# Kernel optimization log

Measured on AMD Instinct MI355X. Metric: run time of the kernel, lower is better.

The kernel has to match this reference:

```python
import jax, jax.numpy as jnp
import numpy as np

B, S, F, H, P, O = 512, 336, 16, 256, 48, 1

def _gru_cell(x, h, Wih, Whh, bih, bhh):
    # torch GRU gate order: r, z, n
    gx = x @ Wih.T + bih            # [B, 3H]
    gh = h @ Whh.T + bhh            # [B, 3H]
    rx, zx, nx = jnp.split(gx, 3, axis=-1)
    rh, zh, nh = jnp.split(gh, 3, axis=-1)
    r = jax.nn.sigmoid(rx + rh)
    z = jax.nn.sigmoid(zx + zh)
    n = jnp.tanh(nx + r * nh)
    return (1.0 - z) * n + z * h

def setup_inputs() -> dict:
    key = jax.random.key(0)
    ks = jax.random.split(key, 12)
    s = lambda *sh: 1.0 / np.sqrt(sh[-1])
    d = {}
    d["xb"] = jax.random.normal(ks[0], (B, S, F), dtype=jnp.float32)
    # encoder GRU (1 layer, unidirectional)
    d["enc_Wih"] = jax.random.normal(ks[1], (3 * H, F), dtype=jnp.float32) * s(F)
    d["enc_Whh"] = jax.random.normal(ks[2], (3 * H, H), dtype=jnp.float32) * s(H)
    d["enc_bih"] = jnp.zeros((3 * H,), dtype=jnp.float32)
    d["enc_bhh"] = jnp.zeros((3 * H,), dtype=jnp.float32)
    # attention linear: (H + F) -> S
    d["att_W"] = jax.random.normal(ks[3], (S, H + F), dtype=jnp.float32) * s(H + F)
    d["att_b"] = jnp.zeros((S,), dtype=jnp.float32)
    # decoder GRUCell: input H, hidden H
    d["dec_Wih"] = jax.random.normal(ks[4], (3 * H, H), dtype=jnp.float32) * s(H)
    d["dec_Whh"] = jax.random.normal(ks[5], (3 * H, H), dtype=jnp.float32) * s(H)
    d["dec_bih"] = jnp.zeros((3 * H,), dtype=jnp.float32)
    d["dec_bhh"] = jnp.zeros((3 * H,), dtype=jnp.float32)
    # decoder output: H -> F
    d["out_W"] = jax.random.normal(ks[6], (F, H), dtype=jnp.float32) * s(H)
    d["out_b"] = jnp.zeros((F,), dtype=jnp.float32)
    # final linear: F -> O
    d["lin_W"] = jax.random.normal(ks[7], (O, F), dtype=jnp.float32) * s(F)
    d["lin_b"] = jnp.zeros((O,), dtype=jnp.float32)
    return d

def reference(xb, enc_Wih, enc_Whh, enc_bih, enc_bhh, att_W, att_b,
              dec_Wih, dec_Whh, dec_bih, dec_bhh, out_W, out_b, lin_W, lin_b):
    # ---- encoder: GRU over time ----
    h0 = jnp.zeros((B, H), dtype=xb.dtype)
    xs = jnp.swapaxes(xb, 0, 1)  # [S, B, F]

    def enc_step(h, x):
        h2 = _gru_cell(x, h, enc_Wih, enc_Whh, enc_bih, enc_bhh)
        return h2, h2

    enc_hidden, enc_out = jax.lax.scan(enc_step, h0, xs)
    enc_out = jnp.swapaxes(enc_out, 0, 1)  # [B, S, H]

    # ---- decoder: per-step attention + GRUCell + output proj ----
    y0 = xb[:, -1, :]  # [B, F]

    def dec_step(carry, _):
        h, y = carry
        att_in = jnp.concatenate([h, y], axis=1)          # [B, H+F]
        attn = jax.nn.softmax(att_in @ att_W.T + att_b, axis=-1)  # [B, S]
        combine = jnp.einsum('bs,bsh->bh', attn, enc_out)  # [B, H]
        h2 = _gru_cell(combine, h, dec_Wih, dec_Whh, dec_bih, dec_bhh)
        out = h2 @ out_W.T + out_b                         # [B, F]
        return (h2, out), out

    _, outs = jax.lax.scan(dec_step, (enc_hidden, y0), None, length=P)  # [P, B, F]
    outs = jnp.swapaxes(outs, 0, 1)                        # [B, P, F]
    outs = outs @ lin_W.T + lin_b                          # [B, P, O]
    return outs.squeeze(-1)                                # [B, P]
```

## Files before the change

kernel.cpp:

```cpp
#include <hip/hip_runtime.h>
#include <cstdint>
#include <cstddef>

#define B_ 512
#define S_ 336
#define F_ 16
#define H_ 256
#define P_ 48

typedef __bf16 bhalf;
typedef __attribute__((ext_vector_type(8))) __bf16 bhalf8;
typedef __attribute__((ext_vector_type(4))) float f32x4;

#define MFMA16(A, Bv, C) __builtin_amdgcn_mfma_f32_16x16x32_bf16((A), (Bv), (C), 0, 0, 0)

__device__ __forceinline__ float fastrcp(float x) { return __builtin_amdgcn_rcpf(x); }
__device__ __forceinline__ float sigm(float x) { return fastrcp(1.0f + __expf(-x)); }
__device__ __forceinline__ float tanh_f(float x) { return 2.0f * fastrcp(1.0f + __expf(-2.0f * x)) - 1.0f; }

__device__ __forceinline__ bhalf u16_to_bf(unsigned int u) {
  return __builtin_bit_cast(__bf16, (unsigned short)u);
}
__device__ __forceinline__ unsigned short bf_to_u16(bhalf b) {
  return __builtin_bit_cast(unsigned short, b);
}

__device__ __forceinline__ bhalf8 bzero8() {
  bhalf8 v;
#pragma unroll
  for (int j = 0; j < 8; ++j) v[j] = (bhalf)0.0f;
  return v;
}

__global__ __launch_bounds__(128, 1) void enc_kernel(
    const float* __restrict__ Whh, const float* __restrict__ Wih,
    const float* __restrict__ bih, const float* __restrict__ bhh,
    const float* __restrict__ xb,
    bhalf* __restrict__ enc_out,
    float* __restrict__ hcur,
    unsigned int* __restrict__ hpack,
    unsigned int* __restrict__ flags)
{
  const int tid  = threadIdx.x;
  const int lane = tid & 63;
  const int wv   = tid >> 6;
  const int ncol = lane & 15;
  const int quad = lane >> 4;

  const int blk = blockIdx.x;
  const int g   = (blk & 7) * 4 + (blk >> 6);
  const int w   = (blk >> 3) & 7;
  const int b0  = g * 16;
  const int iw0 = w * 32;
  const int i0  = iw0 + wv * 16;

  bhalf8 bWh[3][9], bWl[3][9];
#pragma unroll
  for (int gg = 0; gg < 3; ++gg) {
    const int jrow = gg * 256 + i0 + ncol;
#pragma unroll
    for (int kt = 0; kt < 9; ++kt) {
      bhalf8 vh = bzero8(), vl = bzero8();
      if (kt < 8) {
        const float* src = Whh + (size_t)jrow * 256 + kt * 32 + quad * 8;
#pragma unroll
        for (int j = 0; j < 8; ++j) {
          const float v = src[j];
          const bhalf h = (bhalf)v;
          vh[j] = h;
          vl[j] = (bhalf)(v - (float)h);
        }
      } else if (quad < 2) {
        const float* src = Wih + (size_t)jrow * 16 + quad * 8;
#pragma unroll
        for (int j = 0; j < 8; ++j) {
          const float v = src[j];
          const bhalf h = (bhalf)v;
          vh[j] = h;
          vl[j] = (bhalf)(v - (float)h);
        }
      }
      bWh[gg][kt] = vh;
      bWl[gg][kt] = vl;
    }
  }

  const int jr = i0 + ncol;
  const float bR  = bih[jr]       + bhh[jr];
  const float bZ  = bih[256 + jr] + bhh[256 + jr];
  const float bNx = bih[512 + jr];
  const float bNh = bhh[512 + jr];

  const int bA = b0 + ncol;
  const int kA = quad * 8;

  float hold[4] = {0.0f, 0.0f, 0.0f, 0.0f};

  for (int t = 0; t < S_; ++t) {
    bhalf8 xh = bzero8(), xl = bzero8();
    if (quad < 2) {
      const float* xp = xb + ((size_t)bA * S_ + t) * F_ + quad * 8;
#pragma unroll
      for (int j = 0; j < 8; ++j) {
        const float v = __builtin_nontemporal_load(xp + j);
        const bhalf h = (bhalf)v;
        xh[j] = h;
        xl[j] = (bhalf)(v - (float)h);
      }
    }

    f32x4 aR0 = {0,0,0,0}, aR1 = {0,0,0,0}, aR2 = {0,0,0,0};
    f32x4 aZ0 = {0,0,0,0}, aZ1 = {0,0,0,0}, aZ2 = {0,0,0,0};
    f32x4 aN0 = {0,0,0,0}, aN1 = {0,0,0,0}, aN2 = {0,0,0,0};
    f32x4 aNx = {0,0,0,0};

    aR0 = MFMA16(xh, bWh[0][8], aR0);
    aR1 = MFMA16(xh, bWl[0][8], aR1);
    aR2 = MFMA16(xl, bWh[0][8], aR2);
    aZ0 = MFMA16(xh, bWh[1][8], aZ0);
    aZ1 = MFMA16(xh, bWl[1][8], aZ1);
    aZ2 = MFMA16(xl, bWh[1][8], aZ2);
    aNx = MFMA16(xh, bWh[2][8], aNx);
    aNx = MFMA16(xh, bWl[2][8], aNx);
    aNx = MFMA16(xl, bWh[2][8], aNx);

    if (t > 0) {
      const unsigned int* fp = &flags[g * 8 + (lane & 7)];
      while (__hip_atomic_load(fp, __ATOMIC_RELAXED, __HIP_MEMORY_SCOPE_AGENT) <
             (unsigned int)t)
        __builtin_amdgcn_s_sleep(1);

      const int slot = (t - 1) & 1;
      const unsigned long long* hp64 =
          (const unsigned long long*)(hpack + ((size_t)slot * B_ + bA) * H_ + kA);

      unsigned long long wbuf[32];
#pragma unroll
      for (int i = 0; i < 32; ++i)
        wbuf[i] = __hip_atomic_load(hp64 + (i >> 2) * 16 + (i & 3),
                                    __ATOMIC_RELAXED, __HIP_MEMORY_SCOPE_AGENT);

#pragma unroll
      for (int kt = 0; kt < 8; ++kt) {
        bhalf8 Ah, Al;
#pragma unroll
        for (int j2 = 0; j2 < 4; ++j2) {
          const unsigned long long w2 = wbuf[kt * 4 + j2];
          Ah[2 * j2]     = u16_to_bf((unsigned int)w2);
          Al[2 * j2]     = u16_to_bf((unsigned int)(w2 >> 16));
          Ah[2 * j2 + 1] = u16_to_bf((unsigned int)(w2 >> 32));
          Al[2 * j2 + 1] = u16_to_bf((unsigned int)(w2 >> 48));
        }
        aR0 = MFMA16(Ah, bWh[0][kt], aR0);
        aR1 = MFMA16(Ah, bWl[0][kt], aR1);
        aR2 = MFMA16(Al, bWh[0][kt], aR2);
        aZ0 = MFMA16(Ah, bWh[1][kt], aZ0);
        aZ1 = MFMA16(Ah, bWl[1][kt], aZ1);
        aZ2 = MFMA16(Al, bWh[1][kt], aZ2);
        aN0 = MFMA16(Ah, bWh[2][kt], aN0);
        aN1 = MFMA16(Ah, bWl[2][kt], aN1);
        aN2 = MFMA16(Al, bWh[2][kt], aN2);
      }
    }

    const int iL = i0 + ncol;
    bhalf his[4];
#pragma unroll
    for (int r = 0; r < 4; ++r) {
      const float sR  = aR0[r] + aR1[r] + aR2[r] + bR;
      const float sZ  = aZ0[r] + aZ1[r] + aZ2[r] + bZ;
      const float nhv = aN0[r] + aN1[r] + aN2[r] + bNh;
      const float nxv = aNx[r] + bNx;
      const float rr = sigm(sR);
      const float zz = sigm(sZ);
      const float nn = tanh_f(nxv + rr * nhv);
      const float h2 = (1.0f - zz) * nn + zz * hold[r];
      hold[r] = h2;
      his[r] = (bhalf)h2;
      const bhalf lo = (bhalf)(h2 - (float)his[r]);
      const int bb = b0 + quad * 4 + r;
      const unsigned int wrd =
          (unsigned int)bf_to_u16(his[r]) | ((unsigned int)bf_to_u16(lo) << 16);
      __hip_atomic_store(&hpack[((size_t)(t & 1) * B_ + bb) * H_ + iL], wrd,
                         __ATOMIC_RELAXED, __HIP_MEMORY_SCOPE_AGENT);
    }

    __syncthreads();
    if (tid == 0) {
      __hip_atomic_store(&flags[g * 8 + w], (unsigned int)(t + 1),
                         __ATOMIC_RELAXED, __HIP_MEMORY_SCOPE_AGENT);
    }

#pragma unroll
    for (int r = 0; r < 4; ++r) {
      const int bb = b0 + quad * 4 + r;
      __builtin_nontemporal_store(his[r], enc_out + ((size_t)bb * S_ + t) * H_ + iL);
    }
  }

#pragma unroll
  for (int r = 0; r < 4; ++r)
    hcur[(size_t)(b0 + quad * 4 + r) * H_ + i0 + ncol] = hold[r];
}

__global__ __launch_bounds__(256) void wpack_kernel(const float* __restrict__ Whh,
                                                    const float* __restrict__ Wih,
                                                    bhalf* __restrict__ wbT) {
  const int idx = blockIdx.x * 256 + threadIdx.x;
  if (idx >= 64 * 768 * 8) return;
  const int j = idx & 7;
  const int row = (idx >> 3) % 768;
  const int k8 = idx / (768 * 8);
  const int k = k8 * 8 + j;
  const float v = (k < 256) ? Whh[(size_t)row * 256 + k]
                            : Wih[(size_t)row * 256 + (k - 256)];
  wbT[idx] = (bhalf)v;
}

__global__ __launch_bounds__(256) void apack_kernel(const float* __restrict__ attW,
                                                    bhalf* __restrict__ abT) {
  const int idx = blockIdx.x * 256 + threadIdx.x;
  if (idx >= 36 * 336 * 8) return;
  const int j = idx & 7;
  const int s = (idx >> 3) % 336;
  const int k8 = idx / (8 * 336);
  const int k = k8 * 8 + j;
  abT[idx] = (k < 272) ? (bhalf)attW[(size_t)s * 272 + k] : (bhalf)0.0f;
}

__global__ __launch_bounds__(256) void dec_kernel(
    const bhalf* __restrict__ wbT,
    const bhalf* __restrict__ abT,
    const float* __restrict__ attb,
    const float* __restrict__ bih, const float* __restrict__ bhh,
    const float* __restrict__ outW, const float* __restrict__ outb,
    const float* __restrict__ linW, const float* __restrict__ linb,
    const bhalf* __restrict__ enc_out, const float* __restrict__ hcur,
    const float* __restrict__ xb, float* __restrict__ dout)
{
  __shared__ __align__(16) bhalf encL[126 * 256];
  __shared__ __align__(16) float hybuf[2][288];
  __shared__ __align__(16) float cL[256];
  __shared__ float sc[S_];
  __shared__ float pC[8][32][9];
  __shared__ float red[8];
  const int tid  = threadIdx.x;
  const int lane = tid & 63;
  const int wv   = tid >> 6;
  const int b    = blockIdx.x;
  const int jj   = tid;
  const int cg   = tid & 31;
  const int ck   = tid >> 5;
  const int s2ok = tid < 80;
  const int f_o  = tid >> 4;
  const int q_o  = tid & 15;

  {
    const bhalf8* src = (const bhalf8*)(enc_out + (size_t)b * S_ * H_);
    bhalf8* dst = (bhalf8*)encL;
    for (int it = tid; it < 126 * 32; it += 256) dst[it] = src[it];
  }

  hybuf[0][tid] = hcur[(size_t)b * H_ + tid];
  if (tid < 16) {
    hybuf[0][256 + tid] = xb[((size_t)b * S_ + (S_ - 1)) * F_ + tid];
    hybuf[1][256 + tid] = 0.0f;
  } else if (tid < 32) {
    hybuf[0][256 + tid] = 0.0f;
    hybuf[1][256 + tid] = 0.0f;
  }

  const float bRv  = bih[jj]       + bhh[jj];
  const float bZv  = bih[256 + jj] + bhh[256 + jj];
  const float bNxv = bih[512 + jj];
  const float bNhv = bhh[512 + jj];

  const float ab1 = attb[tid];
  const float ab2 = s2ok ? attb[tid + 256] : 0.0f;

  f32x4 ow[4];
  {
    const float* wrp = outW + (size_t)f_o * H_ + q_o * 16;
#pragma unroll
    for (int jv = 0; jv < 4; ++jv) ow[jv] = *(const f32x4*)(wrp + jv * 4);
  }
  const float outb_f = outb[f_o];
  const float linw_t = (tid < 16) ? linW[tid] : 0.0f;
  const float linb0  = linb[0];

  const bhalf* epC = enc_out + ((size_t)b * S_ + ck * 42) * H_ + cg * 8;
  const bhalf* epL = encL + (size_t)(ck * 42) * H_ + cg * 8;
  __syncthreads();

  for (int p = 0; p < P_; ++p) {
    float* hc = hybuf[p & 1];
    float* hn = hybuf[(p & 1) ^ 1];

    float v1, v2 = -3.0e38f;
    {
      float d0 = 0, d1 = 0, d2 = 0, d3 = 0;
#pragma unroll 4
      for (int k8 = 0; k8 < 36; ++k8) {
        const bhalf8 q = *(const bhalf8*)(abT + ((size_t)k8 * S_ + tid) * 8);
        const float* v = hc + k8 * 8;
        d0 += (float)q[0] * v[0] + (float)q[4] * v[4];
        d1 += (float)q[1] * v[1] + (float)q[5] * v[5];
        d2 += (float)q[2] * v[2] + (float)q[6] * v[6];
        d3 += (float)q[3] * v[3] + (float)q[7] * v[7];
      }
      v1 = d0 + d1 + d2 + d3 + ab1;
    }
    if (s2ok) {
      float d0 = 0, d1 = 0, d2 = 0, d3 = 0;
#pragma unroll 4
      for (int k8 = 0; k8 < 36; ++k8) {
        const bhalf8 q = *(const bhalf8*)(abT + ((size_t)k8 * S_ + tid + 256) * 8);
        const float* v = hc + k8 * 8;
        d0 += (float)q[0] * v[0] + (float)q[4] * v[4];
        d1 += (float)q[1] * v[1] + (float)q[5] * v[5];
        d2 += (float)q[2] * v[2] + (float)q[6] * v[6];
        d3 += (float)q[3] * v[3] + (float)q[7] * v[7];
      }
      v2 = d0 + d1 + d2 + d3 + ab2;
    }

    float m = fmaxf(v1, v2);
#pragma unroll
    for (int o = 32; o > 0; o >>= 1) m = fmaxf(m, __shfl_xor(m, o, 64));
    if (lane == 0) red[wv] = m;
    __syncthreads();
    const float mx = fmaxf(fmaxf(red[0], red[1]), fmaxf(red[2], red[3]));
    const float e1 = __expf(v1 - mx);
    sc[tid] = e1;
    float e2 = 0.0f;
    if (s2ok) { e2 = __expf(v2 - mx); sc[tid + 256] = e2; }
    float sum = e1 + e2;
#pragma unroll
    for (int o = 32; o > 0; o >>= 1) sum += __shfl_xor(sum, o, 64);
    if (lane == 0) red[4 + wv] = sum;
    __syncthreads();
    const float inv = fastrcp(red[4] + red[5] + red[6] + red[7]);

    {
      float a0 = 0, a1 = 0, a2 = 0, a3 = 0, a4 = 0, a5 = 0, a6 = 0, a7 = 0;
      const float* scrow = sc + ck * 42;
      if (ck < 3) {
#pragma unroll 6
        for (int s5 = 0; s5 < 42; ++s5) {
          const bhalf8 v = *(const bhalf8*)(epL + (size_t)s5 * H_);
          const float wgt = scrow[s5];
          a0 += wgt * (float)v[0];
          a1 += wgt * (float)v[1];
          a2 += wgt * (float)v[2];
          a3 += wgt * (float)v[3];
          a4 += wgt * (float)v[4];
          a5 += wgt * (float)v[5];
          a6 += wgt * (float)v[6];
          a7 += wgt * (float)v[7];
        }
      } else {
#pragma unroll 6
        for (int s5 = 0; s5 < 42; ++s5) {
          const bhalf8 v = *(const bhalf8*)(epC + (size_t)s5 * H_);
          const float wgt = scrow[s5];
          a0 += wgt * (float)v[0];
          a1 += wgt * (float)v[1];
          a2 += wgt * (float)v[2];
          a3 += wgt * (float)v[3];
          a4 += wgt * (float)v[4];
          a5 += wgt * (float)v[5];
          a6 += wgt * (float)v[6];
          a7 += wgt * (float)v[7];
        }
      }
      float* pp = pC[ck][cg];
      pp[0] = a0; pp[1] = a1; pp[2] = a2; pp[3] = a3;
      pp[4] = a4; pp[5] = a5; pp[6] = a6; pp[7] = a7;
    }
    __syncthreads();

    float r0 = 0, r1 = 0, z0 = 0, z1 = 0, nh0 = 0, nh1 = 0, nx0 = 0, nx1 = 0;
    {
      const int gg = jj >> 3, j = jj & 7;
      float ssum = 0.0f;
#pragma unroll
      for (int c = 0; c < 8; ++c) ssum += pC[c][gg][j];
      cL[jj] = ssum * inv;
    }
#pragma unroll 4
    for (int k8 = 0; k8 < 32; ++k8) {
      const bhalf* base = wbT + ((size_t)k8 * 768) * 8;
      const bhalf8 qR = *(const bhalf8*)(base + (size_t)jj * 8);
      const bhalf8 qZ = *(const bhalf8*)(base + (size_t)(256 + jj) * 8);
      const bhalf8 qN = *(const bhalf8*)(base + (size_t)(512 + jj) * 8);
      const float* v = hc + k8 * 8;
      r0 += (float)qR[0]*v[0] + (float)qR[2]*v[2] + (float)qR[4]*v[4] + (float)qR[6]*v[6];
      r1 += (float)qR[1]*v[1] + (float)qR[3]*v[3] + (float)qR[5]*v[5] + (float)qR[7]*v[7];
      z0 += (float)qZ[0]*v[0] + (float)qZ[2]*v[2] + (float)qZ[4]*v[4] + (float)qZ[6]*v[6];
      z1 += (float)qZ[1]*v[1] + (float)qZ[3]*v[3] + (float)qZ[5]*v[5] + (float)qZ[7]*v[7];
      nh0 += (float)qN[0]*v[0] + (float)qN[2]*v[2] + (float)qN[4]*v[4] + (float)qN[6]*v[6];
      nh1 += (float)qN[1]*v[1] + (float)qN[3]*v[3] + (float)qN[5]*v[5] + (float)qN[7]*v[7];
    }
    __syncthreads();
#pragma unroll 4
    for (int k8 = 32; k8 < 64; ++k8) {
      const bhalf* base = wbT + ((size_t)k8 * 768) * 8;
      const bhalf8 qR = *(const bhalf8*)(base + (size_t)jj * 8);
      const bhalf8 qZ = *(const bhalf8*)(base + (size_t)(256 + jj) * 8);
      const bhalf8 qN = *(const bhalf8*)(base + (size_t)(512 + jj) * 8);
      const float* v = cL + (k8 - 32) * 8;
      r0 += (float)qR[0]*v[0] + (float)qR[2]*v[2] + (float)qR[4]*v[4] + (float)qR[6]*v[6];
      r1 += (float)qR[1]*v[1] + (float)qR[3]*v[3] + (float)qR[5]*v[5] + (float)qR[7]*v[7];
      z0 += (float)qZ[0]*v[0] + (float)qZ[2]*v[2] + (float)qZ[4]*v[4] + (float)qZ[6]*v[6];
      z1 += (float)qZ[1]*v[1] + (float)qZ[3]*v[3] + (float)qZ[5]*v[5] + (float)qZ[7]*v[7];
      nx0 += (float)qN[0]*v[0] + (float)qN[2]*v[2] + (float)qN[4]*v[4] + (float)qN[6]*v[6];
      nx1 += (float)qN[1]*v[1] + (float)qN[3]*v[3] + (float)qN[5]*v[5] + (float)qN[7]*v[7];
    }
    {
      const float sR = r0 + r1 + bRv;
      const float sZ = z0 + z1 + bZv;
      const float nh = nh0 + nh1 + bNhv;
      const float nx = nx0 + nx1 + bNxv;
      const float rr = 1.0f / (1.0f + __expf(-sR));
      const float zz = 1.0f / (1.0f + __expf(-sZ));
      const float nn = tanhf(nx + rr * nh);
      hn[jj] = (1.0f - zz) * nn + zz * hc[jj];
    }
    __syncthreads();

    {
      const float* hv = hn + q_o * 16;
      float a0 = 0, a1 = 0, a2 = 0, a3 = 0;
#pragma unroll
      for (int jv = 0; jv < 4; ++jv) {
        const f32x4 h4 = *(const f32x4*)(hv + jv * 4);
        a0 += ow[jv][0] * h4[0]; a1 += ow[jv][1] * h4[1];
        a2 += ow[jv][2] * h4[2]; a3 += ow[jv][3] * h4[3];
      }
      float a = a0 + a1 + a2 + a3;
      a += __shfl_xor(a, 1, 64); a += __shfl_xor(a, 2, 64);
      a += __shfl_xor(a, 4, 64); a += __shfl_xor(a, 8, 64);
      if (q_o == 0) hn[256 + f_o] = a + outb_f;
    }
    __syncthreads();
    if (tid < 16) {
      float v = hn[256 + tid] * linw_t;
      v += __shfl_xor(v, 1, 64); v += __shfl_xor(v, 2, 64);
      v += __shfl_xor(v, 4, 64); v += __shfl_xor(v, 8, 64);
      if (tid == 0) dout[(size_t)b * P_ + p] = v + linb0;
    }
  }
}

extern "C" void kernel_launch(void* const* d_in, const int* in_sizes, int n_in,
                              void* d_out, int out_size, void* d_ws, size_t ws_size,
                              hipStream_t stream)
{
  (void)in_sizes; (void)n_in; (void)out_size;
  const float* xb      = (const float*)d_in[0];
  const float* enc_Wih = (const float*)d_in[1];
  const float* enc_Whh = (const float*)d_in[2];
  const float* enc_bih = (const float*)d_in[3];
  const float* enc_bhh = (const float*)d_in[4];
  const float* att_W   = (const float*)d_in[5];
  const float* att_b   = (const float*)d_in[6];
  const float* dec_Wih = (const float*)d_in[7];
  const float* dec_Whh = (const float*)d_in[8];
  const float* dec_bih = (const float*)d_in[9];
  const float* dec_bhh = (const float*)d_in[10];
  const float* out_W   = (const float*)d_in[11];
  const float* out_b   = (const float*)d_in[12];
  const float* lin_W   = (const float*)d_in[13];
  const float* lin_b   = (const float*)d_in[14];
  float* dout = (float*)d_out;

  char* ws = (char*)d_ws;
  const size_t off_enc = 0;
  const size_t off_hp  = off_enc + (size_t)B_ * S_ * H_ * 2;
  const size_t off_hc  = off_hp + (size_t)2 * B_ * H_ * 4;
  const size_t off_wb  = off_hc + (size_t)B_ * H_ * 4;
  const size_t off_ab  = off_wb + (size_t)64 * 768 * 8 * 2;
  const size_t off_fl  = off_ab + (size_t)36 * 336 * 8 * 2;
  const size_t need    = off_fl + 32 * 8 * sizeof(unsigned int);
  if (ws_size < need) return;

  bhalf* enc_out      = (bhalf*)(ws + off_enc);
  unsigned int* hpack = (unsigned int*)(ws + off_hp);
  float* hcur         = (float*)(ws + off_hc);
  bhalf* wbT          = (bhalf*)(ws + off_wb);
  bhalf* abT          = (bhalf*)(ws + off_ab);
  unsigned int* flags = (unsigned int*)(ws + off_fl);

  (void)hipMemsetAsync(flags, 0, 32 * 8 * sizeof(unsigned int), stream);
  wpack_kernel<<<(64 * 768 * 8 + 255) / 256, 256, 0, stream>>>(dec_Whh, dec_Wih, wbT);
  apack_kernel<<<(36 * 336 * 8 + 255) / 256, 256, 0, stream>>>(att_W, abT);
  enc_kernel<<<256, 128, 0, stream>>>(enc_Whh, enc_Wih, enc_bih, enc_bhh, xb,
                                      enc_out, hcur, hpack, flags);
  dec_kernel<<<B_, 256, 0, stream>>>(wbT, abT, att_b, dec_bih, dec_bhh,
                                     out_W, out_b, lin_W, lin_b,
                                     enc_out, hcur, xb, dout);
}
```

Baseline: 2.997 ms.

## Process two batch rows per decoder block to reuse weight loads

The decoder kernel now handles two batch rows per 256-thread block, launching B/2 blocks. Each bf16 weight vector loaded for the attention and GRU matvecs is applied to both rows, halving global weight traffic per row. In exchange, the LDS cache of encoder outputs shrinks from 126 to 84 sequence positions per row, so more of enc_out is read from global memory each step. Register pressure also rises, and only 256 blocks are launched, which may underfill the GPU's compute units.

New measurement: 3.073 ms. 1.03x slower.

```diff
diff --git a/kernel.cpp b/kernel.cpp
--- a/kernel.cpp
+++ b/kernel.cpp
@@ -238,16 +238,18 @@
     const bhalf* __restrict__ enc_out, const float* __restrict__ hcur,
     const float* __restrict__ xb, float* __restrict__ dout)
 {
-  __shared__ __align__(16) bhalf encL[126 * 256];
-  __shared__ __align__(16) float hybuf[2][288];
-  __shared__ __align__(16) float cL[256];
-  __shared__ float sc[S_];
-  __shared__ float pC[8][32][9];
-  __shared__ float red[8];
+  __shared__ __align__(16) bhalf encL[2][84 * 256];
+  __shared__ __align__(16) float hybuf[2][2][288];
+  __shared__ __align__(16) float cL[2][256];
+  __shared__ float sc[2][S_];
+  __shared__ float pC[2][8][32][9];
+  __shared__ float red[16];
   const int tid  = threadIdx.x;
   const int lane = tid & 63;
   const int wv   = tid >> 6;
-  const int b    = blockIdx.x;
+  const int blk  = blockIdx.x;
+  const int bR0  = blk * 2;
+  const int bR1  = blk * 2 + 1;
   const int jj   = tid;
   const int cg   = tid & 31;
   const int ck   = tid >> 5;
@@ -255,19 +257,25 @@
   const int f_o  = tid >> 4;
   const int q_o  = tid & 15;
 
-  {
-    const bhalf8* src = (const bhalf8*)(enc_out + (size_t)b * S_ * H_);
-    bhalf8* dst = (bhalf8*)encL;
-    for (int it = tid; it < 126 * 32; it += 256) dst[it] = src[it];
+  for (int it = tid; it < 2 * 84 * 32; it += 256) {
+    const int ri  = it / (84 * 32);
+    const int idx = it - ri * (84 * 32);
+    ((bhalf8*)encL)[it] =
+        ((const bhalf8*)(enc_out + (size_t)(bR0 + ri) * S_ * H_))[idx];
   }
 
-  hybuf[0][tid] = hcur[(size_t)b * H_ + tid];
+  hybuf[0][0][tid] = hcur[(size_t)bR0 * H_ + tid];
+  hybuf[0][1][tid] = hcur[(size_t)bR1 * H_ + tid];
   if (tid < 16) {
-    hybuf[0][256 + tid] = xb[((size_t)b * S_ + (S_ - 1)) * F_ + tid];
-    hybuf[1][256 + tid] = 0.0f;
+    hybuf[0][0][256 + tid] = xb[((size_t)bR0 * S_ + (S_ - 1)) * F_ + tid];
+    hybuf[0][1][256 + tid] = xb[((size_t)bR1 * S_ + (S_ - 1)) * F_ + tid];
+    hybuf[1][0][256 + tid] = 0.0f;
+    hybuf[1][1][256 + tid] = 0.0f;
   } else if (tid < 32) {
-    hybuf[0][256 + tid] = 0.0f;
-    hybuf[1][256 + tid] = 0.0f;
+    hybuf[0][0][256 + tid] = 0.0f;
+    hybuf[0][1][256 + tid] = 0.0f;
+    hybuf[1][0][256 + tid] = 0.0f;
+    hybuf[1][1][256 + tid] = 0.0f;
   }
 
   const float bRv  = bih[jj]       + bhh[jj];
@@ -285,107 +293,131 @@
     for (int jv = 0; jv < 4; ++jv) ow[jv] = *(const f32x4*)(wrp + jv * 4);
   }
   const float outb_f = outb[f_o];
-  const float linw_t = (tid < 16) ? linW[tid] : 0.0f;
+  const float linw_t = (tid < 32) ? linW[tid & 15] : 0.0f;
   const float linb0  = linb[0];
 
-  const bhalf* epC = enc_out + ((size_t)b * S_ + ck * 42) * H_ + cg * 8;
-  const bhalf* epL = encL + (size_t)(ck * 42) * H_ + cg * 8;
   __syncthreads();
 
   for (int p = 0; p < P_; ++p) {
-    float* hc = hybuf[p & 1];
-    float* hn = hybuf[(p & 1) ^ 1];
-
-    float v1, v2 = -3.0e38f;
+    float* hcA = hybuf[p & 1][0];
+    float* hcB = hybuf[p & 1][1];
+    float* hnA = hybuf[(p & 1) ^ 1][0];
+    float* hnB = hybuf[(p & 1) ^ 1][1];
+
+    float vA1, vB1, vA2 = -3.0e38f, vB2 = -3.0e38f;
     {
-      float d0 = 0, d1 = 0, d2 = 0, d3 = 0;
+      float dA0 = 0, dA1 = 0, dA2 = 0, dA3 = 0;
+      float dB0 = 0, dB1 = 0, dB2 = 0, dB3 = 0;
 #pragma unroll 4
       for (int k8 = 0; k8 < 36; ++k8) {
         const bhalf8 q = *(const bhalf8*)(abT + ((size_t)k8 * S_ + tid) * 8);
-        const float* v = hc + k8 * 8;
-        d0 += (float)q[0] * v[0] + (float)q[4] * v[4];
-        d1 += (float)q[1] * v[1] + (float)q[5] * v[5];
-        d2 += (float)q[2] * v[2] + (float)q[6] * v[6];
-        d3 += (float)q[3] * v[3] + (float)q[7] * v[7];
-      }
-      v1 = d0 + d1 + d2 + d3 + ab1;
+        const float* vA = hcA + k8 * 8;
+        const float* vB = hcB + k8 * 8;
+        dA0 += (float)q[0] * vA[0] + (float)q[4] * vA[4];
+        dA1 += (float)q[1] * vA[1] + (float)q[5] * vA[5];
+        dA2 += (float)q[2] * vA[2] + (float)q[6] * vA[6];
+        dA3 += (float)q[3] * vA[3] + (float)q[7] * vA[7];
+        dB0 += (float)q[0] * vB[0] + (float)q[4] * vB[4];
+        dB1 += (float)q[1] * vB[1] + (float)q[5] * vB[5];
+        dB2 += (float)q[2] * vB[2] + (float)q[6] * vB[6];
+        dB3 += (float)q[3] * vB[3] + (float)q[7] * vB[7];
+      }
+      vA1 = dA0 + dA1 + dA2 + dA3 + ab1;
+      vB1 = dB0 + dB1 + dB2 + dB3 + ab1;
     }
     if (s2ok) {
-      float d0 = 0, d1 = 0, d2 = 0, d3 = 0;
+      float dA0 = 0, dA1 = 0, dA2 = 0, dA3 = 0;
+      float dB0 = 0, dB1 = 0, dB2 = 0, dB3 = 0;
 #pragma unroll 4
       for (int k8 = 0; k8 < 36; ++k8) {
         const bhalf8 q = *(const bhalf8*)(abT + ((size_t)k8 * S_ + tid + 256) * 8);
-        const float* v = hc + k8 * 8;
-        d0 += (float)q[0] * v[0] + (float)q[4] * v[4];
-        d1 += (float)q[1] * v[1] + (float)q[5] * v[5];
-        d2 += (float)q[2] * v[2] + (float)q[6] * v[6];
-        d3 += (float)q[3] * v[3] + (float)q[7] * v[7];
-      }
-      v2 = d0 + d1 + d2 + d3 + ab2;
-    }
-
-    float m = fmaxf(v1, v2);
-#pragma unroll
-    for (int o = 32; o > 0; o >>= 1) m = fmaxf(m, __shfl_xor(m, o, 64));
-    if (lane == 0) red[wv] = m;
-    __syncthreads();
-    const float mx = fmaxf(fmaxf(red[0], red[1]), fmaxf(red[2], red[3]));
-    const float e1 = __expf(v1 - mx);
-    sc[tid] = e1;
-    float e2 = 0.0f;
-    if (s2ok) { e2 = __expf(v2 - mx); sc[tid + 256] = e2; }
-    float sum = e1 + e2;
-#pragma unroll
-    for (int o = 32; o > 0; o >>= 1) sum += __shfl_xor(sum, o, 64);
-    if (lane == 0) red[4 + wv] = sum;
-    __syncthreads();
-    const float inv = fastrcp(red[4] + red[5] + red[6] + red[7]);
-
-    {
+        const float* vA = hcA + k8 * 8;
+        const float* vB = hcB + k8 * 8;
+        dA0 += (float)q[0] * vA[0] + (float)q[4] * vA[4];
+        dA1 += (float)q[1] * vA[1] + (float)q[5] * vA[5];
+        dA2 += (float)q[2] * vA[2] + (float)q[6] * vA[6];
+        dA3 += (float)q[3] * vA[3] + (float)q[7] * vA[7];
+        dB0 += (float)q[0] * vB[0] + (float)q[4] * vB[4];
+        dB1 += (float)q[1] * vB[1] + (float)q[5] * vB[5];
+        dB2 += (float)q[2] * vB[2] + (float)q[6] * vB[6];
+        dB3 += (float)q[3] * vB[3] + (float)q[7] * vB[7];
+      }
+      vA2 = dA0 + dA1 + dA2 + dA3 + ab2;
+      vB2 = dB0 + dB1 + dB2 + dB3 + ab2;
+    }
+
+    float mA = fmaxf(vA1, vA2), mB = fmaxf(vB1, vB2);
+#pragma unroll
+    for (int o = 32; o > 0; o >>= 1) {
+      mA = fmaxf(mA, __shfl_xor(mA, o, 64));
+      mB = fmaxf(mB, __shfl_xor(mB, o, 64));
+    }
+    if (lane == 0) { red[wv] = mA; red[4 + wv] = mB; }
+    __syncthreads();
+    const float mxA = fmaxf(fmaxf(red[0], red[1]), fmaxf(red[2], red[3]));
+    const float mxB = fmaxf(fmaxf(red[4], red[5]), fmaxf(red[6], red[7]));
+    const float eA1 = __expf(vA1 - mxA);
+    const float eB1 = __expf(vB1 - mxB);
+    sc[0][tid] = eA1;
+    sc[1][tid] = eB1;
+    float eA2 = 0.0f, eB2 = 0.0f;
+    if (s2ok) {
+      eA2 = __expf(vA2 - mxA); sc[0][tid + 256] = eA2;
+      eB2 = __expf(vB2 - mxB); sc[1][tid + 256] = eB2;
+    }
+    float sumA = eA1 + eA2, sumB = eB1 + eB2;
+#pragma unroll
+    for (int o = 32; o > 0; o >>= 1) {
+      sumA += __shfl_xor(sumA, o, 64);
+      sumB += __shfl_xor(sumB, o, 64);
+    }
+    if (lane == 0) { red[8 + wv] = sumA; red[12 + wv] = sumB; }
+    __syncthreads();
+    const float invA = fastrcp(red[8] + red[9] + red[10] + red[11]);
+    const float invB = fastrcp(red[12] + red[13] + red[14] + red[15]);
+
+#pragma unroll
+    for (int ri = 0; ri < 2; ++ri) {
       float a0 = 0, a1 = 0, a2 = 0, a3 = 0, a4 = 0, a5 = 0, a6 = 0, a7 = 0;
-      const float* scrow = sc + ck * 42;
-      if (ck < 3) {
+      const float* scr = sc[ri] + ck * 42;
+      if (ck < 2) {
+        const bhalf* eb = encL[ri] + (size_t)(ck * 42) * H_ + cg * 8;
 #pragma unroll 6
         for (int s5 = 0; s5 < 42; ++s5) {
-          const bhalf8 v = *(const bhalf8*)(epL + (size_t)s5 * H_);
-          const float wgt = scrow[s5];
-          a0 += wgt * (float)v[0];
-          a1 += wgt * (float)v[1];
-          a2 += wgt * (float)v[2];
-          a3 += wgt * (float)v[3];
-          a4 += wgt * (float)v[4];
-          a5 += wgt * (float)v[5];
-          a6 += wgt * (float)v[6];
-          a7 += wgt * (float)v[7];
+          const bhalf8 v = *(const bhalf8*)(eb + (size_t)s5 * H_);
+          const float w = scr[s5];
+          a0 += w * (float)v[0]; a1 += w * (float)v[1];
+          a2 += w * (float)v[2]; a3 += w * (float)v[3];
+          a4 += w * (float)v[4]; a5 += w * (float)v[5];
+          a6 += w * (float)v[6]; a7 += w * (float)v[7];
         }
       } else {
+        const bhalf* eb = enc_out + ((size_t)(bR0 + ri) * S_ + ck * 42) * H_ + cg * 8;
 #pragma unroll 6
         for (int s5 = 0; s5 < 42; ++s5) {
-          const bhalf8 v = *(const bhalf8*)(epC + (size_t)s5 * H_);
-          const float wgt = scrow[s5];
-          a0 += wgt * (float)v[0];
-          a1 += wgt * (float)v[1];
-          a2 += wgt * (float)v[2];
-          a3 += wgt * (float)v[3];
-          a4 += wgt * (float)v[4];
-          a5 += wgt * (float)v[5];
-          a6 += wgt * (float)v[6];
-          a7 += wgt * (float)v[7];
+          const bhalf8 v = *(const bhalf8*)(eb + (size_t)s5 * H_);
+          const float w = scr[s5];
+          a0 += w * (float)v[0]; a1 += w * (float)v[1];
+          a2 += w * (float)v[2]; a3 += w * (float)v[3];
+          a4 += w * (float)v[4]; a5 += w * (float)v[5];
+          a6 += w * (float)v[6]; a7 += w * (float)v[7];
         }
       }
-      float* pp = pC[ck][cg];
+      float* pp = pC[ri][ck][cg];
       pp[0] = a0; pp[1] = a1; pp[2] = a2; pp[3] = a3;
       pp[4] = a4; pp[5] = a5; pp[6] = a6; pp[7] = a7;
     }
     __syncthreads();
 
-    float r0 = 0, r1 = 0, z0 = 0, z1 = 0, nh0 = 0, nh1 = 0, nx0 = 0, nx1 = 0;
+    float rA0 = 0, rA1 = 0, zA0 = 0, zA1 = 0, nhA0 = 0, nhA1 = 0, nxA0 = 0, nxA1 = 0;
+    float rB0 = 0, rB1 = 0, zB0 = 0, zB1 = 0, nhB0 = 0, nhB1 = 0, nxB0 = 0, nxB1 = 0;
     {
       const int gg = jj >> 3, j = jj & 7;
-      float ssum = 0.0f;
-#pragma unroll
-      for (int c = 0; c < 8; ++c) ssum += pC[c][gg][j];
-      cL[jj] = ssum * inv;
+      float sA = 0.0f, sB = 0.0f;
+#pragma unroll
+      for (int c = 0; c < 8; ++c) { sA += pC[0][c][gg][j]; sB += pC[1][c][gg][j]; }
+      cL[0][jj] = sA * invA;
+      cL[1][jj] = sB * invB;
     }
 #pragma unroll 4
     for (int k8 = 0; k8 < 32; ++k8) {
@@ -393,13 +425,20 @@
       const bhalf8 qR = *(const bhalf8*)(base + (size_t)jj * 8);
       const bhalf8 qZ = *(const bhalf8*)(base + (size_t)(256 + jj) * 8);
       const bhalf8 qN = *(const bhalf8*)(base + (size_t)(512 + jj) * 8);
-      const float* v = hc + k8 * 8;
-      r0 += (float)qR[0]*v[0] + (float)qR[2]*v[2] + (float)qR[4]*v[4] + (float)qR[6]*v[6];
-      r1 += (float)qR[1]*v[1] + (float)qR[3]*v[3] + (float)qR[5]*v[5] + (float)qR[7]*v[7];
-      z0 += (float)qZ[0]*v[0] + (float)qZ[2]*v[2] + (float)qZ[4]*v[4] + (float)qZ[6]*v[6];
-      z1 += (float)qZ[1]*v[1] + (float)qZ[3]*v[3] + (float)qZ[5]*v[5] + (float)qZ[7]*v[7];
-      nh0 += (float)qN[0]*v[0] + (float)qN[2]*v[2] + (float)qN[4]*v[4] + (float)qN[6]*v[6];
-      nh1 += (float)qN[1]*v[1] + (float)qN[3]*v[3] + (float)qN[5]*v[5] + (float)qN[7]*v[7];
+      const float* vA = hcA + k8 * 8;
+      const float* vB = hcB + k8 * 8;
+      rA0 += (float)qR[0]*vA[0] + (float)qR[2]*vA[2] + (float)qR[4]*vA[4] + (float)qR[6]*vA[6];
+      rA1 += (float)qR[1]*vA[1] + (float)qR[3]*vA[3] + (float)qR[5]*vA[5] + (float)qR[7]*vA[7];
+      zA0 += (float)qZ[0]*vA[0] + (float)qZ[2]*vA[2] + (float)qZ[4]*vA[4] + (float)qZ[6]*vA[6];
+      zA1 += (float)qZ[1]*vA[1] + (float)qZ[3]*vA[3] + (float)qZ[5]*vA[5] + (float)qZ[7]*vA[7];
+      nhA0 += (float)qN[0]*vA[0] + (float)qN[2]*vA[2] + (float)qN[4]*vA[4] + (float)qN[6]*vA[6];
+      nhA1 += (float)qN[1]*vA[1] + (float)qN[3]*vA[3] + (float)qN[5]*vA[5] + (float)qN[7]*vA[7];
+      rB0 += (float)qR[0]*vB[0] + (float)qR[2]*vB[2] + (float)qR[4]*vB[4] + (float)qR[6]*vB[6];
+      rB1 += (float)qR[1]*vB[1] + (float)qR[3]*vB[3] + (float)qR[5]*vB[5] + (float)qR[7]*vB[7];
+      zB0 += (float)qZ[0]*vB[0] + (float)qZ[2]*vB[2] + (float)qZ[4]*vB[4] + (float)qZ[6]*vB[6];
+      zB1 += (float)qZ[1]*vB[1] + (float)qZ[3]*vB[3] + (float)qZ[5]*vB[5] + (float)qZ[7]*vB[7];
+      nhB0 += (float)qN[0]*vB[0] + (float)qN[2]*vB[2] + (float)qN[4]*vB[4] + (float)qN[6]*vB[6];
+      nhB1 += (float)qN[1]*vB[1] + (float)qN[3]*vB[3] + (float)qN[5]*vB[5] + (float)qN[7]*vB[7];
     }
     __syncthreads();
 #pragma unroll 4
@@ -408,46 +447,69 @@
       const bhalf8 qR = *(const bhalf8*)(base + (size_t)jj * 8);
       const bhalf8 qZ = *(const bhalf8*)(base + (size_t)(256 + jj) * 8);
       const bhalf8 qN = *(const bhalf8*)(base + (size_t)(512 + jj) * 8);
-      const float* v = cL + (k8 - 32) * 8;
-      r0 += (float)qR[0]*v[0] + (float)qR[2]*v[2] + (float)qR[4]*v[4] + (float)qR[6]*v[6];
-      r1 += (float)qR[1]*v[1] + (float)qR[3]*v[3] + (float)qR[5]*v[5] + (float)qR[7]*v[7];
-      z0 += (float)qZ[0]*v[0] + (float)qZ[2]*v[2] + (float)qZ[4]*v[4] + (float)qZ[6]*v[6];
-      z1 += (float)qZ[1]*v[1] + (float)qZ[3]*v[3] + (float)qZ[5]*v[5] + (float)qZ[7]*v[7];
-      nx0 += (float)qN[0]*v[0] + (float)qN[2]*v[2] + (float)qN[4]*v[4] + (float)qN[6]*v[6];
-      nx1 += (float)qN[1]*v[1] + (float)qN[3]*v[3] + (float)qN[5]*v[5] + (float)qN[7]*v[7];
+      const float* vA = cL[0] + (k8 - 32) * 8;
+      const float* vB = cL[1] + (k8 - 32) * 8;
+      rA0 += (float)qR[0]*vA[0] + (float)qR[2]*vA[2] + (float)qR[4]*vA[4] + (float)qR[6]*vA[6];
+      rA1 += (float)qR[1]*vA[1] + (float)qR[3]*vA[3] + (float)qR[5]*vA[5] + (float)qR[7]*vA[7];
+      zA0 += (float)qZ[0]*vA[0] + (float)qZ[2]*vA[2] + (float)qZ[4]*vA[4] + (float)qZ[6]*vA[6];
+      zA1 += (float)qZ[1]*vA[1] + (float)qZ[3]*vA[3] + (float)qZ[5]*vA[5] + (float)qZ[7]*vA[7];
+      nxA0 += (float)qN[0]*vA[0] + (float)qN[2]*vA[2] + (float)qN[4]*vA[4] + (float)qN[6]*vA[6];
+      nxA1 += (float)qN[1]*vA[1] + (float)qN[3]*vA[3] + (float)qN[5]*vA[5] + (float)qN[7]*vA[7];
+      rB0 += (float)qR[0]*vB[0] + (float)qR[2]*vB[2] + (float)qR[4]*vB[4] + (float)qR[6]*vB[6];
+      rB1 += (float)qR[1]*vB[1] + (float)qR[3]*vB[3] + (float)qR[5]*vB[5] + (float)qR[7]*vB[7];
+      zB0 += (float)qZ[0]*vB[0] + (float)qZ[2]*vB[2] + (float)qZ[4]*vB[4] + (float)qZ[6]*vB[6];
+      zB1 += (float)qZ[1]*vB[1] + (float)qZ[3]*vB[3] + (float)qZ[5]*vB[5] + (float)qZ[7]*vB[7];
+      nxB0 += (float)qN[0]*vB[0] + (float)qN[2]*vB[2] + (float)qN[4]*vB[4] + (float)qN[6]*vB[6];
+      nxB1 += (float)qN[1]*vB[1] + (float)qN[3]*vB[3] + (float)qN[5]*vB[5] + (float)qN[7]*vB[7];
     }
     {
-      const float sR = r0 + r1 + bRv;
-      const float sZ = z0 + z1 + bZv;
-      const float nh = nh0 + nh1 + bNhv;
-      const float nx = nx0 + nx1 + bNxv;
-      const float rr = 1.0f / (1.0f + __expf(-sR));
-      const float zz = 1.0f / (1.0f + __expf(-sZ));
-      const float nn = tanhf(nx + rr * nh);
-      hn[jj] = (1.0f - zz) * nn + zz * hc[jj];
+      const float sRA = rA0 + rA1 + bRv;
+      const float sZA = zA0 + zA1 + bZv;
+      const float nhA = nhA0 + nhA1 + bNhv;
+      const float nxA = nxA0 + nxA1 + bNxv;
+      const float rrA = 1.0f / (1.0f + __expf(-sRA));
+      const float zzA = 1.0f / (1.0f + __expf(-sZA));
+      const float nnA = tanhf(nxA + rrA * nhA);
+      hnA[jj] = (1.0f - zzA) * nnA + zzA * hcA[jj];
+
+      const float sRB = rB0 + rB1 + bRv;
+      const float sZB = zB0 + zB1 + bZv;
+      const float nhB = nhB0 + nhB1 + bNhv;
+      const float nxB = nxB0 + nxB1 + bNxv;
+      const float rrB = 1.0f / (1.0f + __expf(-sRB));
+      const float zzB = 1.0f / (1.0f + __expf(-sZB));
+      const float nnB = tanhf(nxB + rrB * nhB);
+      hnB[jj] = (1.0f - zzB) * nnB + zzB * hcB[jj];
     }
     __syncthreads();
 
     {
-      const float* hv = hn + q_o * 16;
-      float a0 = 0, a1 = 0, a2 = 0, a3 = 0;
+      const float* hvA = hnA + q_o * 16;
+      const float* hvB = hnB + q_o * 16;
+      float aA = 0, aB = 0;
 #pragma unroll
       for (int jv = 0; jv < 4; ++jv) {
-        const f32x4 h4 = *(const f32x4*)(hv + jv * 4);
-        a0 += ow[jv][0] * h4[0]; a1 += ow[jv][1] * h4[1];
-        a2 += ow[jv][2] * h4[2]; a3 += ow[jv][3] * h4[3];
-      }
-      float a = a0 + a1 + a2 + a3;
-      a += __shfl_xor(a, 1, 64); a += __shfl_xor(a, 2, 64);
-      a += __shfl_xor(a, 4, 64); a += __shfl_xor(a, 8, 64);
-      if (q_o == 0) hn[256 + f_o] = a + outb_f;
-    }
-    __syncthreads();
-    if (tid < 16) {
-      float v = hn[256 + tid] * linw_t;
+        const f32x4 hA4 = *(const f32x4*)(hvA + jv * 4);
+        const f32x4 hB4 = *(const f32x4*)(hvB + jv * 4);
+        aA += ow[jv][0]*hA4[0] + ow[jv][1]*hA4[1] + ow[jv][2]*hA4[2] + ow[jv][3]*hA4[3];
+        aB += ow[jv][0]*hB4[0] + ow[jv][1]*hB4[1] + ow[jv][2]*hB4[2] + ow[jv][3]*hB4[3];
+      }
+      aA += __shfl_xor(aA, 1, 64); aA += __shfl_xor(aA, 2, 64);
+      aA += __shfl_xor(aA, 4, 64); aA += __shfl_xor(aA, 8, 64);
+      aB += __shfl_xor(aB, 1, 64); aB += __shfl_xor(aB, 2, 64);
+      aB += __shfl_xor(aB, 4, 64); aB += __shfl_xor(aB, 8, 64);
+      if (q_o == 0) {
+        hnA[256 + f_o] = aA + outb_f;
+        hnB[256 + f_o] = aB + outb_f;
+      }
+    }
+    __syncthreads();
+    if (tid < 32) {
+      const int l16 = tid & 15, ri = tid >> 4;
+      float v = hybuf[(p & 1) ^ 1][ri][256 + l16] * linw_t;
       v += __shfl_xor(v, 1, 64); v += __shfl_xor(v, 2, 64);
       v += __shfl_xor(v, 4, 64); v += __shfl_xor(v, 8, 64);
-      if (tid == 0) dout[(size_t)b * P_ + p] = v + linb0;
+      if (l16 == 0) dout[(size_t)(bR0 + ri) * P_ + p] = v + linb0;
     }
   }
 }
@@ -496,7 +558,7 @@
   apack_kernel<<<(36 * 336 * 8 + 255) / 256, 256, 0, stream>>>(att_W, abT);
   enc_kernel<<<256, 128, 0, stream>>>(enc_Whh, enc_Wih, enc_bih, enc_bhh, xb,
                                       enc_out, hcur, hpack, flags);
-  dec_kernel<<<B_, 256, 0, stream>>>(wbT, abT, att_b, dec_bih, dec_bhh,
-                                     out_W, out_b, lin_W, lin_b,
-                                     enc_out, hcur, xb, dout);
-}
+  dec_kernel<<<B_ / 2, 256, 0, stream>>>(wbT, abT, att_b, dec_bih, dec_bhh,
+                                         out_W, out_b, lin_W, lin_b,
+                                         enc_out, hcur, xb, dout);
+}
```
